# Kernel optimization log

Hardware: AMD Instinct MI355X
Metric: run time of the kernel (lower is better)

Reference implementation:

```python
import jax, jax.numpy as jnp
import numpy as np

S = 9                      # spiral length
V = [8192, 4096, 2048, 1024, 512]  # verts per level, finest -> latent


def grid_sample_bilinear(feat, grid):
    # feat [B,C,H,W], grid [B,P,2] in [-1,1]; bilinear, align_corners=True
    B, C, H, W = feat.shape
    x = (grid[..., 0] + 1.0) * 0.5 * (W - 1)
    y = (grid[..., 1] + 1.0) * 0.5 * (H - 1)
    x0 = jnp.floor(x); y0 = jnp.floor(y)
    wx = x - x0; wy = y - y0
    x0i = jnp.clip(x0.astype(jnp.int32), 0, W - 1)
    x1i = jnp.clip(x0.astype(jnp.int32) + 1, 0, W - 1)
    y0i = jnp.clip(y0.astype(jnp.int32), 0, H - 1)
    y1i = jnp.clip(y0.astype(jnp.int32) + 1, 0, H - 1)
    featf = feat.reshape(B, C, H * W).transpose(0, 2, 1)  # [B,HW,C]
    def gat(yi, xi):
        return jnp.take_along_axis(featf, (yi * W + xi)[..., None], axis=1)  # [B,P,C]
    w00 = ((1 - wy) * (1 - wx))[..., None]
    w01 = ((1 - wy) * wx)[..., None]
    w10 = (wy * (1 - wx))[..., None]
    w11 = (wy * wx)[..., None]
    return gat(y0i, x0i) * w00 + gat(y0i, x1i) * w01 + gat(y1i, x0i) * w10 + gat(y1i, x1i) * w11


def pool(x, row, col, val):
    # sparse mesh upsample: gather cols, scale, scatter-add into rows
    n_out = row.shape[0] // 3
    g = x[:, col, :] * val[None, :, None]                       # [B,nnz,C]
    return jnp.zeros((x.shape[0], n_out, x.shape[-1]), x.dtype).at[:, row, :].add(g)


def dsconv(x, idx, wd, wp, b):
    # depthwise-separable spiral conv: gather spiral ring, depthwise over S, pointwise mix
    g = x[:, idx]                                # [B,N,S,C]
    dw = jnp.einsum('bnsc,sc->bnc', g, wd)       # depthwise over spiral dim
    return jnp.einsum('bnc,co->bno', dw, wp) + b # pointwise


def _forward(uv, feat, upsample, s0, s1, s2, s3,
             row0, col0, val0, row1, col1, val1, row2, col2, val2, row3, col3, val3,
             wd0, wp0, b0, wd1, wp1, b1, wd2, wp2, b2, wd3, wp3, b3, wdh, wph, bh):
    uvc = jnp.clip((uv - 0.5) * 2.0, -1.0, 1.0)
    x = grid_sample_bilinear(feat, uvc)           # [B,P,C]  (torch: [B,C,P] then permute)
    x = jnp.einsum('vp,bpc->bvc', upsample, x)    # [B,V4,C] latent mesh features
    x = jax.nn.relu(dsconv(pool(x, row3, col3, val3), s3, wd0, wp0, b0))  # [B,1024,512]
    x = jax.nn.relu(dsconv(pool(x, row2, col2, val2), s2, wd1, wp1, b1))  # [B,2048,256]
    x = jax.nn.relu(dsconv(pool(x, row1, col1, val1), s1, wd2, wp2, b2))  # [B,4096,128]
    x = jax.nn.relu(dsconv(pool(x, row0, col0, val0), s0, wd3, wp3, b3))  # [B,8192,64]
    return dsconv(x, s0, wdh, wph, bh)            # [B,8192,3]


def setup_inputs():
    ks = jax.random.split(jax.random.key(0), 64)
    B, P, C, H, W = 8, 21, 512, 32, 32
    inp = {}
    inp['uv'] = jax.random.uniform(ks[0], (B, P, 2), jnp.float32)
    inp['feat'] = jax.random.normal(ks[1], (B, C, H, W), jnp.float32)
    inp['upsample'] = 0.01 * jnp.ones((V[4], P), jnp.float32)
    for i in range(4):
        inp[f's{i}'] = jax.random.randint(ks[2 + i], (V[i], S), 0, V[i])
    for i in range(4):
        nnz = 3 * V[i]
        inp[f'row{i}'] = jax.random.randint(ks[6 + 3 * i], (nnz,), 0, V[i])
        inp[f'col{i}'] = jax.random.randint(ks[7 + 3 * i], (nnz,), 0, V[i + 1])
        inp[f'val{i}'] = jax.random.uniform(ks[8 + 3 * i], (nnz,), jnp.float32)
    chans = [(512, 512), (512, 256), (256, 128), (128, 64), (64, 3)]
    names = ['0', '1', '2', '3', 'h']
    k = 20
    for (ci, co), nm in zip(chans, names):
        inp[f'wd{nm}'] = 0.1 * jax.random.normal(ks[k], (S, ci), jnp.float32); k += 1
        inp[f'wp{nm}'] = jax.random.normal(ks[k], (ci, co), jnp.float32) * (1.0 / float(np.sqrt(ci))); k += 1
        inp[f'b{nm}'] = jnp.zeros((co,), jnp.float32); k += 1
    return inp


def reference(uv, feat, upsample, s0, s1, s2, s3,
              row0, col0, val0, row1, col1, val1, row2, col2, val2, row3, col3, val3,
              wd0, wp0, b0, wd1, wp1, b1, wd2, wp2, b2, wd3, wp3, b3, wdh, wph, bh):
    return _forward(uv, feat, upsample, s0, s1, s2, s3,
                    row0, col0, val0, row1, col1, val1, row2, col2, val2, row3, col3, val3,
                    wd0, wp0, b0, wd1, wp1, b1, wd2, wp2, b2, wd3, wp3, b3, wdh, wph, bh)
```

## Files before the change

### kernel.cpp

```cpp
#include <hip/hip_runtime.h>

#define B_  8
#define P_  21
#define H_  32
#define W_  32

typedef float f32x4 __attribute__((ext_vector_type(4)));
typedef _Float16 f16x8 __attribute__((ext_vector_type(8)));

struct CsrParams {
  const int*   row[4];
  const int*   col[4];
  const float* val[4];
  int*   cnt[4];
  int*   rowptr[4];
  int*   colsout[4];
  float* valsout[4];
  int    nnz[4];
  int    V[4];
};

__global__ void zero_cnt_kernel(int* p, int n) {
  int i = blockIdx.x * 256 + threadIdx.x;
  if (i < n) p[i] = 0;
}

__global__ void count_kernel(CsrParams p) {
  int l = blockIdx.y;
  int k = blockIdx.x * 256 + threadIdx.x;
  if (k < p.nnz[l]) atomicAdd(&p.cnt[l][p.row[l][k]], 1);
}

__global__ void scan_kernel(CsrParams p) {
  int l = blockIdx.x;
  int V = p.V[l];
  int* cnt = p.cnt[l];
  int* rp  = p.rowptr[l];
  int t = threadIdx.x;
  int chunk = V / 256;
  int base = t * chunk;
  int s = 0;
  for (int i = 0; i < chunk; ++i) s += cnt[base + i];
  __shared__ int sm[256];
  sm[t] = s;
  __syncthreads();
  for (int off = 1; off < 256; off <<= 1) {
    int v = (t >= off) ? sm[t - off] : 0;
    __syncthreads();
    sm[t] += v;
    __syncthreads();
  }
  int run = sm[t] - s;
  for (int i = 0; i < chunk; ++i) {
    int c = cnt[base + i];
    rp[base + i]  = run;
    cnt[base + i] = run;
    run += c;
  }
  if (t == 255) rp[V] = run;
}

__global__ void fill_kernel(CsrParams p) {
  int l = blockIdx.y;
  int k = blockIdx.x * 256 + threadIdx.x;
  if (k < p.nnz[l]) {
    int r = p.row[l][k];
    int pos = atomicAdd(&p.cnt[l][r], 1);
    p.colsout[l][pos] = p.col[l][k];
    p.valsout[l][pos] = p.val[l][k];
  }
}

__global__ void sample_kernel(const float* __restrict__ uv,
                              const float* __restrict__ feat,
                              float* __restrict__ xs) {
  int bp = blockIdx.x;
  int b  = bp / P_;
  float u0 = uv[bp * 2 + 0], u1 = uv[bp * 2 + 1];
  float gx = fminf(fmaxf((u0 - 0.5f) * 2.0f, -1.0f), 1.0f);
  float gy = fminf(fmaxf((u1 - 0.5f) * 2.0f, -1.0f), 1.0f);
  float fx = (gx + 1.0f) * 0.5f * (W_ - 1);
  float fy = (gy + 1.0f) * 0.5f * (H_ - 1);
  float x0f = floorf(fx), y0f = floorf(fy);
  float wx = fx - x0f, wy = fy - y0f;
  int x0 = (int)x0f, y0 = (int)y0f;
  int x0i = min(max(x0, 0), W_ - 1), x1i = min(max(x0 + 1, 0), W_ - 1);
  int y0i = min(max(y0, 0), H_ - 1), y1i = min(max(y0 + 1, 0), H_ - 1);
  float w00 = (1.f - wy) * (1.f - wx), w01 = (1.f - wy) * wx;
  float w10 = wy * (1.f - wx),        w11 = wy * wx;
  for (int c = threadIdx.x; c < 512; c += blockDim.x) {
    const float* fb = feat + ((size_t)(b * 512 + c)) * (H_ * W_);
    float v = fb[y0i * W_ + x0i] * w00 + fb[y0i * W_ + x1i] * w01 +
              fb[y1i * W_ + x0i] * w10 + fb[y1i * W_ + x1i] * w11;
    xs[(size_t)bp * 512 + c] = v;
  }
}

__global__ void upsample_kernel(const float* __restrict__ up,
                                const float* __restrict__ xs,
                                float* __restrict__ xu) {
  int v = blockIdx.x, b = blockIdx.y;
  int c4 = threadIdx.x << 2;
  float4 acc = make_float4(0.f, 0.f, 0.f, 0.f);
  for (int p = 0; p < P_; ++p) {
    float u = up[v * P_ + p];
    const float4 xv = *(const float4*)&xs[((size_t)(b * P_ + p)) * 512 + c4];
    acc.x = fmaf(u, xv.x, acc.x);
    acc.y = fmaf(u, xv.y, acc.y);
    acc.z = fmaf(u, xv.z, acc.z);
    acc.w = fmaf(u, xv.w, acc.w);
  }
  *(float4*)&xu[((size_t)(b * 512 + v)) * 512 + c4] = acc;
}

__global__ __launch_bounds__(256) void pool_kernel(
    const float* __restrict__ x,
    const int* __restrict__ rowptr,
    const int* __restrict__ cols,
    const float* __restrict__ vals,
    float* __restrict__ out,
    int Vout, int Vin, int Cin) {
  const int lpr    = Cin >> 3;
  const int lshift = 31 - __clz(lpr);
  const int rpb    = 256 >> lshift;
  const int lr = threadIdx.x >> lshift;
  const int lc = threadIdx.x & (lpr - 1);
  const int b  = blockIdx.x & 7;
  const int n  = (blockIdx.x >> 3) * rpb + lr;
  const int c8 = lc << 3;
  const float* xb = x + (size_t)b * Vin * Cin + c8;
  int j0 = rowptr[n], j1 = rowptr[n + 1];
  int cnt = j1 - j0;
  float4 a0 = make_float4(0.f, 0.f, 0.f, 0.f);
  float4 a1 = make_float4(0.f, 0.f, 0.f, 0.f);
  if (cnt > 0) {
    int   cc[4];
    float vv[4];
    #pragma unroll
    for (int k = 0; k < 4; ++k) {
      int jj = j0 + ((k < cnt) ? k : 0);
      cc[k] = cols[jj];
      vv[k] = (k < cnt) ? vals[jj] : 0.f;
    }
    #pragma unroll
    for (int k = 0; k < 4; ++k) {
      const float* xr = xb + (size_t)cc[k] * Cin;
      float4 x0 = *(const float4*)xr;
      float4 x1 = *(const float4*)(xr + 4);
      float v = vv[k];
      a0.x = fmaf(v, x0.x, a0.x); a0.y = fmaf(v, x0.y, a0.y);
      a0.z = fmaf(v, x0.z, a0.z); a0.w = fmaf(v, x0.w, a0.w);
      a1.x = fmaf(v, x1.x, a1.x); a1.y = fmaf(v, x1.y, a1.y);
      a1.z = fmaf(v, x1.z, a1.z); a1.w = fmaf(v, x1.w, a1.w);
    }
    for (int j = j0 + 4; j < j1; ++j) {
      float v = vals[j];
      const float* xr = xb + (size_t)cols[j] * Cin;
      float4 x0 = *(const float4*)xr;
      float4 x1 = *(const float4*)(xr + 4);
      a0.x = fmaf(v, x0.x, a0.x); a0.y = fmaf(v, x0.y, a0.y);
      a0.z = fmaf(v, x0.z, a0.z); a0.w = fmaf(v, x0.w, a0.w);
      a1.x = fmaf(v, x1.x, a1.x); a1.y = fmaf(v, x1.y, a1.y);
      a1.z = fmaf(v, x1.z, a1.z); a1.w = fmaf(v, x1.w, a1.w);
    }
  }
  float* op = &out[((size_t)b * Vout + n) * Cin + c8];
  *(float4*)op = a0;
  *(float4*)(op + 4) = a1;
}

__global__ __launch_bounds__(256) void dw_split_kernel(
    const float* __restrict__ xin,
    const int* __restrict__ sidx,
    const float* __restrict__ wd,
    _Float16* __restrict__ a0o,
    _Float16* __restrict__ a1o,
    int Vout, int Cin) {
  const int lpr    = Cin >> 3;
  const int lshift = 31 - __clz(lpr);
  const int rpb    = 256 >> lshift;
  const int lr = threadIdx.x >> lshift;
  const int lc = threadIdx.x & (lpr - 1);
  const int b  = blockIdx.x & 7;
  const int n  = (blockIdx.x >> 3) * rpb + lr;
  const int c8 = lc << 3;
  const float* xb = xin + (size_t)b * Vout * Cin + c8;

  int idx[9];
  #pragma unroll
  for (int s = 0; s < 9; ++s) idx[s] = sidx[n * 9 + s];

  float4 a0 = make_float4(0.f, 0.f, 0.f, 0.f);
  float4 a1 = make_float4(0.f, 0.f, 0.f, 0.f);
  #pragma unroll
  for (int s = 0; s < 9; ++s) {
    const float* xr = xb + (size_t)idx[s] * Cin;
    float4 x0 = *(const float4*)xr;
    float4 x1 = *(const float4*)(xr + 4);
    const float* wr = wd + s * Cin + c8;
    float4 w0 = *(const float4*)wr;
    float4 w1 = *(const float4*)(wr + 4);
    a0.x = fmaf(w0.x, x0.x, a0.x); a0.y = fmaf(w0.y, x0.y, a0.y);
    a0.z = fmaf(w0.z, x0.z, a0.z); a0.w = fmaf(w0.w, x0.w, a0.w);
    a1.x = fmaf(w1.x, x1.x, a1.x); a1.y = fmaf(w1.y, x1.y, a1.y);
    a1.z = fmaf(w1.z, x1.z, a1.z); a1.w = fmaf(w1.w, x1.w, a1.w);
  }

  size_t m = (size_t)b * Vout + n;
  float v[8] = {a0.x, a0.y, a0.z, a0.w, a1.x, a1.y, a1.z, a1.w};
  f16x8 hi, lo;
  #pragma unroll
  for (int i = 0; i < 8; ++i) {
    _Float16 h0 = (_Float16)v[i];
    float r = (v[i] - (float)h0) * 2048.0f;
    hi[i] = h0;
    lo[i] = (_Float16)r;
  }
  *(f16x8*)&a0o[m * Cin + c8] = hi;
  *(f16x8*)&a1o[m * Cin + c8] = lo;
}

struct BsplitParams {
  const float* wp[4];
  int K[4], N[4], off[4];
  _Float16* b0;
  _Float16* b1;
};

__global__ void bsplit_all_kernel(BsplitParams p) {
  int idx = blockIdx.x * 256 + threadIdx.x;
  #pragma unroll
  for (int t = 0; t < 4; ++t) {
    int sz = p.N[t] * p.K[t];
    if (idx < sz) {
      int n = idx / p.K[t], k = idx - n * p.K[t];
      float v = p.wp[t][(size_t)k * p.N[t] + n];
      _Float16 h0 = (_Float16)v;
      float r = (v - (float)h0) * 2048.0f;
      p.b0[p.off[t] + idx] = h0;
      p.b1[p.off[t] + idx] = (_Float16)r;
      return;
    }
    idx -= sz;
  }
}

__global__ __launch_bounds__(256) void gemm_f16x2(
    const _Float16* __restrict__ A0, const _Float16* __restrict__ A1,
    const _Float16* __restrict__ Bt0, const _Float16* __restrict__ Bt1,
    const float* __restrict__ bias, float* __restrict__ C,
    int M, int N, int K) {
  constexpr int RP = 72;
  __shared__ _Float16 As[2][128][RP];
  __shared__ _Float16 Bs[2][64][RP];
  const int tid = threadIdx.x;
  const int bx = blockIdx.x;
  const int xr_ = (bx & 7) * (gridDim.x >> 3) + (bx >> 3);
  const int m0 = xr_ * 128, n0 = blockIdx.y * 64;
  const int wid = tid >> 6, lane = tid & 63;
  const int wr = wid >> 1, wc = wid & 1;
  const int lo = lane & 15, hi = lane >> 4;

  f32x4 accM[4][2], accC[4][2];
  #pragma unroll
  for (int mi = 0; mi < 4; ++mi)
    #pragma unroll
    for (int nj = 0; nj < 2; ++nj) {
      accM[mi][nj] = (f32x4){0.f, 0.f, 0.f, 0.f};
      accC[mi][nj] = (f32x4){0.f, 0.f, 0.f, 0.f};
    }

  const _Float16* gA[2] = {A0, A1};
  const _Float16* gB[2] = {Bt0, Bt1};

  for (int k0 = 0; k0 < K; k0 += 64) {
    #pragma unroll
    for (int p = 0; p < 2; ++p) {
      #pragma unroll
      for (int i = 0; i < 4; ++i) {
        int c = tid + 256 * i;
        int r = c >> 3, k8 = (c & 7) << 3;
        uint4 v = *(const uint4*)(gA[p] + (size_t)(m0 + r) * K + k0 + k8);
        *(uint4*)&As[p][r][k8] = v;
      }
      #pragma unroll
      for (int i = 0; i < 2; ++i) {
        int c = tid + 256 * i;
        int r = c >> 3, k8 = (c & 7) << 3;
        uint4 v = *(const uint4*)(gB[p] + (size_t)(n0 + r) * K + k0 + k8);
        *(uint4*)&Bs[p][r][k8] = v;
      }
    }
    __syncthreads();
    #pragma unroll
    for (int s = 0; s < 2; ++s) {
      const int kk = s * 32 + hi * 8;
      f16x8 af[4][2], bf[2][2];
      #pragma unroll
      for (int mi = 0; mi < 4; ++mi) {
        af[mi][0] = *(const f16x8*)&As[0][wr * 64 + mi * 16 + lo][kk];
        af[mi][1] = *(const f16x8*)&As[1][wr * 64 + mi * 16 + lo][kk];
      }
      #pragma unroll
      for (int nj = 0; nj < 2; ++nj) {
        bf[nj][0] = *(const f16x8*)&Bs[0][wc * 32 + nj * 16 + lo][kk];
        bf[nj][1] = *(const f16x8*)&Bs[1][wc * 32 + nj * 16 + lo][kk];
      }
      #pragma unroll
      for (int mi = 0; mi < 4; ++mi)
        #pragma unroll
        for (int nj = 0; nj < 2; ++nj) {
          accM[mi][nj] = __builtin_amdgcn_mfma_f32_16x16x32_f16(
              af[mi][0], bf[nj][0], accM[mi][nj], 0, 0, 0);
          accC[mi][nj] = __builtin_amdgcn_mfma_f32_16x16x32_f16(
              af[mi][0], bf[nj][1], accC[mi][nj], 0, 0, 0);
          accC[mi][nj] = __builtin_amdgcn_mfma_f32_16x16x32_f16(
              af[mi][1], bf[nj][0], accC[mi][nj], 0, 0, 0);
        }
    }
    __syncthreads();
  }

  const float INV = 1.0f / 2048.0f;
  #pragma unroll
  for (int mi = 0; mi < 4; ++mi)
    #pragma unroll
    for (int nj = 0; nj < 2; ++nj) {
      int col = n0 + wc * 32 + nj * 16 + lo;
      float bv = bias[col];
      #pragma unroll
      for (int r = 0; r < 4; ++r) {
        int row = m0 + wr * 64 + mi * 16 + hi * 4 + r;
        float v = accM[mi][nj][r] + accC[mi][nj][r] * INV + bv;
        v = fmaxf(v, 0.f);
        C[(size_t)row * N + col] = v;
      }
    }
}

__global__ __launch_bounds__(256) void head_fused_kernel(
    const float* __restrict__ x,
    const int* __restrict__ sidx,
    const float* __restrict__ wdh,
    const float* __restrict__ wph,
    const float* __restrict__ bh,
    float* __restrict__ out) {
  const int bid  = blockIdx.x;
  const int b    = bid & 7;
  const int wid  = threadIdx.x >> 6;
  const int lane = threadIdx.x & 63;
  const int n    = (bid >> 3) * 4 + wid;
  const float* xb = x + (size_t)b * 8192 * 64 + lane;

  int idx[9];
  #pragma unroll
  for (int s = 0; s < 9; ++s) idx[s] = sidx[n * 9 + s];

  float acc = 0.f;
  #pragma unroll
  for (int s = 0; s < 9; ++s)
    acc = fmaf(wdh[s * 64 + lane], xb[(size_t)idx[s] * 64], acc);

  float a0 = acc * wph[lane * 3 + 0];
  float a1 = acc * wph[lane * 3 + 1];
  float a2 = acc * wph[lane * 3 + 2];
  for (int off = 32; off > 0; off >>= 1) {
    a0 += __shfl_down(a0, off);
    a1 += __shfl_down(a1, off);
    a2 += __shfl_down(a2, off);
  }
  if (lane == 0) {
    size_t row = (size_t)b * 8192 + n;
    out[row * 3 + 0] = a0 + bh[0];
    out[row * 3 + 1] = a1 + bh[1];
    out[row * 3 + 2] = a2 + bh[2];
  }
}

extern "C" void kernel_launch(void* const* d_in, const int* in_sizes, int n_in,
                              void* d_out, int out_size, void* d_ws, size_t ws_size,
                              hipStream_t stream) {
  const float* uv   = (const float*)d_in[0];
  const float* feat = (const float*)d_in[1];
  const float* up   = (const float*)d_in[2];
  const int* sArr[4] = {(const int*)d_in[3], (const int*)d_in[4],
                        (const int*)d_in[5], (const int*)d_in[6]};

  const size_t SLAB = 8ull * 2048 * 512;
  float* Wf = (float*)d_ws;
  float* S0 = Wf;
  float* S1 = Wf + SLAB;
  _Float16* A0 = (_Float16*)(S1 + SLAB);
  _Float16* A1 = A0 + SLAB;
  _Float16* Bt0all = (_Float16*)(S0 + 4500000);
  _Float16* Bt1all = Bt0all + 434176;
  float* xs = (float*)(A1 + SLAB);
  int* ib = (int*)(xs + (size_t)B_ * P_ * 512);

  int Vt[4] = {1024, 2048, 4096, 8192};
  int NZ[4] = {3072, 6144, 12288, 24576};
  int* cnt[4]; int* rp[4]; int* co[4]; float* va[4];
  {
    int* pc = ib;
    for (int t = 0; t < 4; ++t) { cnt[t] = pc; pc += Vt[t]; }
    for (int t = 0; t < 4; ++t) { rp[t] = pc; pc += Vt[t] + 1; }
    for (int t = 0; t < 4; ++t) { co[t] = pc; pc += NZ[t]; }
    float* pv = (float*)pc;
    for (int t = 0; t < 4; ++t) { va[t] = pv; pv += NZ[t]; }
  }

  CsrParams cp;
  for (int t = 0; t < 4; ++t) {
    int i = 3 - t;
    cp.row[t] = (const int*)d_in[7 + 3 * i];
    cp.col[t] = (const int*)d_in[8 + 3 * i];
    cp.val[t] = (const float*)d_in[9 + 3 * i];
    cp.cnt[t] = cnt[t]; cp.rowptr[t] = rp[t];
    cp.colsout[t] = co[t]; cp.valsout[t] = va[t];
    cp.nnz[t] = NZ[t]; cp.V[t] = Vt[t];
  }

  zero_cnt_kernel<<<60, 256, 0, stream>>>(ib, 15360);
  count_kernel<<<dim3(96, 4), 256, 0, stream>>>(cp);
  scan_kernel<<<4, 256, 0, stream>>>(cp);
  fill_kernel<<<dim3(96, 4), 256, 0, stream>>>(cp);

  sample_kernel<<<B_ * P_, 256, 0, stream>>>(uv, feat, xs);
  upsample_kernel<<<dim3(512, B_), 128, 0, stream>>>(up, xs, S0);

  struct Stg { int Vin, Vout, Cin, Cout; const int* s; const float *wd, *wp, *bias; };
  Stg st[4] = {
    {512, 1024, 512, 512, sArr[3], (const float*)d_in[19], (const float*)d_in[20], (const float*)d_in[21]},
    {1024, 2048, 512, 256, sArr[2], (const float*)d_in[22], (const float*)d_in[23], (const float*)d_in[24]},
    {2048, 4096, 256, 128, sArr[1], (const float*)d_in[25], (const float*)d_in[26], (const float*)d_in[27]},
    {4096, 8192, 128, 64, sArr[0], (const float*)d_in[28], (const float*)d_in[29], (const float*)d_in[30]},
  };

  BsplitParams bp;
  int boff = 0;
  for (int t = 0; t < 4; ++t) {
    bp.wp[t] = st[t].wp;
    bp.K[t] = st[t].Cin; bp.N[t] = st[t].Cout;
    bp.off[t] = boff;
    boff += st[t].Cin * st[t].Cout;
  }
  bp.b0 = Bt0all; bp.b1 = Bt1all;
  bsplit_all_kernel<<<(boff + 255) / 256, 256, 0, stream>>>(bp);

  for (int t = 0; t < 4; ++t) {
    int rpb = 2048 / st[t].Cin;
    pool_kernel<<<8 * (st[t].Vout / rpb), 256, 0, stream>>>(
        S0, rp[t], co[t], va[t], S1, st[t].Vout, st[t].Vin, st[t].Cin);
    dw_split_kernel<<<8 * (st[t].Vout / rpb), 256, 0, stream>>>(
        S1, st[t].s, st[t].wd, A0, A1, st[t].Vout, st[t].Cin);
    int M = B_ * st[t].Vout;
    gemm_f16x2<<<dim3(M / 128, st[t].Cout / 64), 256, 0, stream>>>(
        A0, A1, Bt0all + bp.off[t], Bt1all + bp.off[t],
        st[t].bias, S0, M, st[t].Cout, st[t].Cin);
  }

  head_fused_kernel<<<8 * (8192 / 4), 256, 0, stream>>>(
      S0, sArr[0], (const float*)d_in[31], (const float*)d_in[32],
      (const float*)d_in[33], (float*)d_out);
}
```

Measured before the change: 278.6 us.

## Load GEMM tiles directly into LDS with XOR-swizzled producer layouts

The GEMM now uses global_load_lds to copy A and B tiles straight from global memory into shared memory, skipping the register round-trip. Because this direct-to-LDS path cannot add row padding, the producer kernels (the activation split and the weight split) write their f16 outputs with a column-chunk XOR swizzle keyed on the row. The MFMA fragment reads apply the matching swizzle, which is meant to avoid LDS bank conflicts. This ties the global data layout to the GEMM's tile geometry, and correctness depends on the swizzle being consistent across all three kernels.

```diff
diff --git a/kernel.cpp b/kernel.cpp
--- a/kernel.cpp
+++ b/kernel.cpp
@@ -7,6 +7,12 @@
 
 typedef float f32x4 __attribute__((ext_vector_type(4)));
 typedef _Float16 f16x8 __attribute__((ext_vector_type(8)));
+
+__device__ __forceinline__ void gload_lds16(const _Float16* g, _Float16* l) {
+  __builtin_amdgcn_global_load_lds(
+      (const __attribute__((address_space(1))) void*)g,
+      (__attribute__((address_space(3))) void*)l, 16, 0, 0);
+}
 
 struct CsrParams {
   const int*   row[4];
@@ -216,8 +222,9 @@
     hi[i] = h0;
     lo[i] = (_Float16)r;
   }
-  *(f16x8*)&a0o[m * Cin + c8] = hi;
-  *(f16x8*)&a1o[m * Cin + c8] = lo;
+  const int c8s = (lc ^ (n & 7)) << 3;
+  *(f16x8*)&a0o[m * Cin + c8s] = hi;
+  *(f16x8*)&a1o[m * Cin + c8s] = lo;
 }
 
 struct BsplitParams {
@@ -233,12 +240,14 @@
   for (int t = 0; t < 4; ++t) {
     int sz = p.N[t] * p.K[t];
     if (idx < sz) {
-      int n = idx / p.K[t], k = idx - n * p.K[t];
+      int K = p.K[t];
+      int n = idx / K, k = idx - n * K;
       float v = p.wp[t][(size_t)k * p.N[t] + n];
       _Float16 h0 = (_Float16)v;
       float r = (v - (float)h0) * 2048.0f;
-      p.b0[p.off[t] + idx] = h0;
-      p.b1[p.off[t] + idx] = (_Float16)r;
+      int ks = ((((k >> 3) ^ (n & 7)) << 3) | (k & 7));
+      p.b0[p.off[t] + (size_t)n * K + ks] = h0;
+      p.b1[p.off[t] + (size_t)n * K + ks] = (_Float16)r;
       return;
     }
     idx -= sz;
@@ -250,9 +259,8 @@
     const _Float16* __restrict__ Bt0, const _Float16* __restrict__ Bt1,
     const float* __restrict__ bias, float* __restrict__ C,
     int M, int N, int K) {
-  constexpr int RP = 72;
-  __shared__ _Float16 As[2][128][RP];
-  __shared__ _Float16 Bs[2][64][RP];
+  __shared__ _Float16 As[2][128 * 64];
+  __shared__ _Float16 Bs[2][64 * 64];
   const int tid = threadIdx.x;
   const int bx = blockIdx.x;
   const int xr_ = (bx & 7) * (gridDim.x >> 3) + (bx >> 3);
@@ -280,31 +288,35 @@
       for (int i = 0; i < 4; ++i) {
         int c = tid + 256 * i;
         int r = c >> 3, k8 = (c & 7) << 3;
-        uint4 v = *(const uint4*)(gA[p] + (size_t)(m0 + r) * K + k0 + k8);
-        *(uint4*)&As[p][r][k8] = v;
+        gload_lds16(gA[p] + (size_t)(m0 + r) * K + k0 + k8,
+                    &As[p][(c & ~63) * 8]);
       }
       #pragma unroll
       for (int i = 0; i < 2; ++i) {
         int c = tid + 256 * i;
         int r = c >> 3, k8 = (c & 7) << 3;
-        uint4 v = *(const uint4*)(gB[p] + (size_t)(n0 + r) * K + k0 + k8);
-        *(uint4*)&Bs[p][r][k8] = v;
+        gload_lds16(gB[p] + (size_t)(n0 + r) * K + k0 + k8,
+                    &Bs[p][(c & ~63) * 8]);
       }
     }
     __syncthreads();
     #pragma unroll
     for (int s = 0; s < 2; ++s) {
-      const int kk = s * 32 + hi * 8;
+      const int cl = s * 4 + hi;
       f16x8 af[4][2], bf[2][2];
       #pragma unroll
       for (int mi = 0; mi < 4; ++mi) {
-        af[mi][0] = *(const f16x8*)&As[0][wr * 64 + mi * 16 + lo][kk];
-        af[mi][1] = *(const f16x8*)&As[1][wr * 64 + mi * 16 + lo][kk];
+        const int rr = wr * 64 + mi * 16 + lo;
+        const int ko = (cl ^ (rr & 7)) << 3;
+        af[mi][0] = *(const f16x8*)&As[0][rr * 64 + ko];
+        af[mi][1] = *(const f16x8*)&As[1][rr * 64 + ko];
       }
       #pragma unroll
       for (int nj = 0; nj < 2; ++nj) {
-        bf[nj][0] = *(const f16x8*)&Bs[0][wc * 32 + nj * 16 + lo][kk];
-        bf[nj][1] = *(const f16x8*)&Bs[1][wc * 32 + nj * 16 + lo][kk];
+        const int rb = wc * 32 + nj * 16 + lo;
+        const int ko = (cl ^ (rb & 7)) << 3;
+        bf[nj][0] = *(const f16x8*)&Bs[0][rb * 64 + ko];
+        bf[nj][1] = *(const f16x8*)&Bs[1][rb * 64 + ko];
       }
       #pragma unroll
       for (int mi = 0; mi < 4; ++mi)
```

Result: faster. 271.5 us (-2.5%).
